# Kernel tuning notes

Measured on AMD Instinct MI355X. Metric: run time of the kernel, lower is better.

Reference implementation:

```python
import jax, jax.numpy as jnp
import numpy as np

N = 100_000          # nodes (node_shape = [N, D])
D = 64               # node feature dim
E = 3_200_000        # edges (edge_shape = [E, 1]), avg degree 32
GAMMA = 0.5          # registered buffer 'gamma'


def setup_inputs() -> dict:
    key = jax.random.key(0)
    k1, k2, k3, k4 = jax.random.split(key, 4)
    h = jax.random.normal(k1, (N * D,), dtype=jnp.float32)
    e = jax.random.normal(k2, (E,), dtype=jnp.float32)
    x = jnp.concatenate([h, e])                      # flat ODE state [N*D + E]
    src = jax.random.randint(k3, (E,), 0, N, dtype=jnp.int32)
    dst = jax.random.randint(k4, (E,), 0, N, dtype=jnp.int32)
    t = jnp.zeros((1,), dtype=jnp.float32)           # unused by the math
    return {"t": t, "x": x, "src": src, "dst": dst}


def reference(t, x, src, dst):
    # split flat state into node features and edge weights
    h = x[: N * D].reshape(N, D)        # ndata['h']
    e = x[N * D:].reshape(E, 1)         # edata['e']
    h0 = h
    # update_all(u_mul_e('h','e','m'), sum('m','h')):
    # gather source features, scale by edge weight, scatter-sum to dst
    msgs = h[src] * e                                   # [E, D]
    h_agg = jax.ops.segment_sum(msgs, dst, num_segments=N)  # [N, D]
    h_new = h_agg - h0 * GAMMA
    # self.h0 is None -> no residual add
    return jnp.concatenate([h_new.reshape(-1), jnp.zeros((E,), x.dtype)])
```

## Files before the change

kernel.cpp:

```cpp
#include <hip/hip_runtime.h>

#define N_NODES 100000
#define D_FEAT  64
#define N_EDGES 3200000
#define GAMMA   0.5f

#define BSH   7
#define BN    (1 << BSH)
#define NB    ((N_NODES + BN - 1) >> BSH)
#define CH    2048
#define NC    ((N_EDGES + CH - 1) / CH)

#define Z_BLOCKS   782
#define CVT_V4     (N_NODES * D_FEAT / 4)
#define CVT_BLOCKS ((CVT_V4 + 255) / 256)

#define KG_REG   10
#define KG_CAP   4736
#define SRC_MASK 0x1FFFFu

__global__ void __launch_bounds__(256)
p0_kernel(const float* __restrict__ h,
          const int* __restrict__ dst,
          unsigned short* __restrict__ h16,
          unsigned short* __restrict__ mat,
          float* __restrict__ out_edge) {
    __shared__ int hist[NB];
    const int bid = blockIdx.x;
    const int t   = threadIdx.x;
    if (bid < NC) {
        for (int i = t; i < NB; i += 256) hist[i] = 0;
        __syncthreads();
        const int base  = bid * CH;
        const int chcnt = min(N_EDGES - base, CH);
        const int4* dst4 = (const int4*)(dst + base);
        const int nv4 = chcnt >> 2;
#pragma unroll
        for (int j = 0; j < 2; ++j) {
            int i = j * 256 + t;
            if (i < nv4) {
                int4 d = dst4[i];
                __hip_atomic_fetch_add(&hist[d.x >> BSH], 1, __ATOMIC_RELAXED, __HIP_MEMORY_SCOPE_WORKGROUP);
                __hip_atomic_fetch_add(&hist[d.y >> BSH], 1, __ATOMIC_RELAXED, __HIP_MEMORY_SCOPE_WORKGROUP);
                __hip_atomic_fetch_add(&hist[d.z >> BSH], 1, __ATOMIC_RELAXED, __HIP_MEMORY_SCOPE_WORKGROUP);
                __hip_atomic_fetch_add(&hist[d.w >> BSH], 1, __ATOMIC_RELAXED, __HIP_MEMORY_SCOPE_WORKGROUP);
            }
        }
        __syncthreads();
        for (int i = t; i < NB; i += 256)
            mat[bid * NB + i] = (unsigned short)hist[i];
    } else if (bid < NC + Z_BLOCKS) {
        float4* oe4 = (float4*)out_edge;
        const int b2 = bid - NC;
        const float4 z = make_float4(0.f, 0.f, 0.f, 0.f);
#pragma unroll
        for (int j = 0; j < 4; ++j) {
            int i = b2 * 1024 + j * 256 + t;
            if (i < N_EDGES / 4) oe4[i] = z;
        }
    } else {
        int i = (bid - NC - Z_BLOCKS) * 256 + t;
        if (i < CVT_V4) {
            float4 v = ((const float4*)h)[i];
            ushort4 o;
            unsigned u;
            u = __float_as_uint(v.x); o.x = (unsigned short)((u + 0x7fffu + ((u >> 16) & 1u)) >> 16);
            u = __float_as_uint(v.y); o.y = (unsigned short)((u + 0x7fffu + ((u >> 16) & 1u)) >> 16);
            u = __float_as_uint(v.z); o.z = (unsigned short)((u + 0x7fffu + ((u >> 16) & 1u)) >> 16);
            u = __float_as_uint(v.w); o.w = (unsigned short)((u + 0x7fffu + ((u >> 16) & 1u)) >> 16);
            ((ushort4*)h16)[i] = o;
        }
    }
}

__global__ void __launch_bounds__(64)
matscan_kernel(unsigned short* __restrict__ mat,
               int* __restrict__ rowsum) {
    const int b = blockIdx.x;
    const int l = threadIdx.x;
    int carry = 0;
    for (int r = 0; r < (NC + 63) / 64; ++r) {
        int c = r * 64 + l;
        int v = (c < NC) ? (int)mat[c * NB + b] : 0;
        int incl = v;
        for (int s = 1; s < 64; s <<= 1) {
            int u = __shfl_up(incl, s, 64);
            if (l >= s) incl += u;
        }
        if (c < NC) mat[c * NB + b] = (unsigned short)(carry + incl - v);
        carry += __shfl(incl, 63, 64);
    }
    if (l == 0) rowsum[b] = carry;
}

__global__ void __launch_bounds__(512)
bucket_scatter_kernel(const int* __restrict__ src,
                      const int* __restrict__ dst,
                      const float* __restrict__ e,
                      const unsigned short* __restrict__ mat,
                      const int* __restrict__ rowsum,
                      int* __restrict__ offs_g,
                      uint2* __restrict__ recs) {
    __shared__ uint2          stage[CH];
    __shared__ unsigned short bkt[CH];
    __shared__ int hist[NB], ebuf[NB], pos[NB], diff[NB];
    __shared__ int offsL[NB + 1];
    __shared__ int wsum[8];

    const int t    = threadIdx.x;
    const int lane = t & 63;
    const int wid  = t >> 6;
    const int c    = blockIdx.x;
    const int base = c * CH;
    const int chcnt = min(N_EDGES - base, CH);
    const int i0 = 2 * t, i1 = 2 * t + 1;

    for (int i = t; i < NB; i += 512) hist[i] = 0;
    int a  = (i0 < NB) ? rowsum[i0] : 0;
    int d1 = (i1 < NB) ? rowsum[i1] : 0;
    int pair = a + d1, incl = pair;
    for (int s = 1; s < 64; s <<= 1) {
        int u = __shfl_up(incl, s, 64);
        if (lane >= s) incl += u;
    }
    if (lane == 63) wsum[wid] = incl;
    __syncthreads();
    {
        int pre = 0;
        for (int w = 0; w < wid; ++w) pre += wsum[w];
        int excl = pre + incl - pair;
        if (i0 < NB) offsL[i0] = excl;
        if (i1 < NB) offsL[i1] = excl + a;
        if (t == 511) offsL[NB] = pre + incl;
    }
    int dv[4];
#pragma unroll
    for (int j = 0; j < 4; ++j) {
        int i = j * 512 + t;
        if (i < chcnt) {
            dv[j] = dst[base + i];
            __hip_atomic_fetch_add(&hist[dv[j] >> BSH], 1,
                                   __ATOMIC_RELAXED, __HIP_MEMORY_SCOPE_WORKGROUP);
        } else dv[j] = -1;
    }
    __syncthreads();
    int c0 = (i0 < NB) ? hist[i0] : 0;
    int c1 = (i1 < NB) ? hist[i1] : 0;
    int p2 = c0 + c1, incl2 = p2;
    for (int s = 1; s < 64; s <<= 1) {
        int u = __shfl_up(incl2, s, 64);
        if (lane >= s) incl2 += u;
    }
    if (lane == 63) wsum[wid] = incl2;
    __syncthreads();
    {
        int pre = 0;
        for (int w = 0; w < wid; ++w) pre += wsum[w];
        int excl2 = pre + incl2 - p2;
        if (i0 < NB) {
            ebuf[i0] = excl2;
            pos[i0]  = excl2;
            diff[i0] = offsL[i0] + (int)mat[c * NB + i0] - excl2;
        }
        if (i1 < NB) {
            ebuf[i1] = excl2 + c0;
            pos[i1]  = excl2 + c0;
            diff[i1] = offsL[i1] + (int)mat[c * NB + i1] - (excl2 + c0);
        }
    }
    __syncthreads();
#pragma unroll
    for (int j = 0; j < 4; ++j) {
        if (dv[j] >= 0) {
            int gi = base + j * 512 + t;
            int b  = dv[j] >> BSH;
            int p  = __hip_atomic_fetch_add(&pos[b], 1,
                            __ATOMIC_RELAXED, __HIP_MEMORY_SCOPE_WORKGROUP);
            unsigned pk = (unsigned)src[gi] | ((unsigned)(dv[j] & (BN - 1)) << 17);
            stage[p] = make_uint2(pk, __float_as_uint(e[gi]));
            bkt[p]   = (unsigned short)b;
        }
    }
    __syncthreads();
    for (int i = t; i < chcnt; i += 512) {
        recs[diff[bkt[i]] + i] = stage[i];
    }
    if (c == 0) {
        for (int i = t; i <= NB; i += 512) offs_g[i] = offsL[i];
    }
}

__global__ void __launch_bounds__(512)
sort_gather_kernel(const float* __restrict__ h,
                   const unsigned short* __restrict__ h16,
                   const int* __restrict__ offs,
                   const uint2* __restrict__ recs,
                   float* __restrict__ out) {
    __shared__ uint2 kw[KG_CAP];
    __shared__ int hist[BN], ebuf[BN], pos[BN];
    __shared__ int wsum[2];

    const int b    = blockIdx.x;
    const int t    = threadIdx.x;
    const int lane = t & 63;
    const int wid  = t >> 6;
    const int g    = lane >> 3;
    const int sub  = lane & 7;
    const int lo   = offs[b];
    const int cnt  = offs[b + 1] - lo;

    const uint4* __restrict__ hv = (const uint4*)h16;

#define ACC_KW(kx, wx)                                                      \
    {                                                                       \
        uint4 v = hv[((kx) & SRC_MASK) * 8 + sub];                          \
        a0 += __uint_as_float(v.x << 16) * (wx);                            \
        a1 += __uint_as_float(v.x & 0xFFFF0000u) * (wx);                    \
        a2 += __uint_as_float(v.y << 16) * (wx);                            \
        a3 += __uint_as_float(v.y & 0xFFFF0000u) * (wx);                    \
        a4 += __uint_as_float(v.z << 16) * (wx);                            \
        a5 += __uint_as_float(v.z & 0xFFFF0000u) * (wx);                    \
        a6 += __uint_as_float(v.w << 16) * (wx);                            \
        a7 += __uint_as_float(v.w & 0xFFFF0000u) * (wx);                    \
    }

    if (cnt <= KG_CAP) {
        if (t < BN) hist[t] = 0;
        __syncthreads();
        uint2 r[KG_REG];
#pragma unroll
        for (int j = 0; j < KG_REG; ++j) {
            int i = j * 512 + t;
            if (i < cnt) {
                r[j] = recs[lo + i];
                __hip_atomic_fetch_add(&hist[r[j].x >> 17], 1,
                                       __ATOMIC_RELAXED, __HIP_MEMORY_SCOPE_WORKGROUP);
            } else r[j].x = 0xFFFFFFFFu;
        }
        __syncthreads();
        int c = 0, incl = 0;
        if (t < BN) { c = hist[t]; incl = c; }
        for (int s = 1; s < 64; s <<= 1) {
            int u = __shfl_up(incl, s, 64);
            if (lane >= s) incl += u;
        }
        if (t < BN && lane == 63) wsum[wid] = incl;
        __syncthreads();
        if (t < BN) {
            int pre = (wid == 1) ? wsum[0] : 0;
            int exc = pre + incl - c;
            ebuf[t] = exc;
            pos[t]  = exc;
        }
        __syncthreads();
#pragma unroll
        for (int j = 0; j < KG_REG; ++j) {
            if (r[j].x != 0xFFFFFFFFu) {
                int dl = r[j].x >> 17;
                int p  = __hip_atomic_fetch_add(&pos[dl], 1,
                                __ATOMIC_RELAXED, __HIP_MEMORY_SCOPE_WORKGROUP);
                kw[p] = r[j];
            }
        }
        __syncthreads();
        for (int i = 0; i < 16; ++i) {
            const int ln  = wid * 16 + i;
            const int n   = (b << BSH) + ln;
            const int nlo = ebuf[ln];
            const int nhi = pos[ln];
            float a0=0.f,a1=0.f,a2=0.f,a3=0.f,a4=0.f,a5=0.f,a6=0.f,a7=0.f;
            int kk = nlo + g;
            while (kk < nhi) {
                uint2 q0 = kw[kk];
                bool m1 = kk +  8 < nhi;
                bool m2 = kk + 16 < nhi;
                bool m3 = kk + 24 < nhi;
                uint2 q1 = m1 ? kw[kk +  8] : make_uint2(0u, 0u);
                uint2 q2 = m2 ? kw[kk + 16] : make_uint2(0u, 0u);
                uint2 q3 = m3 ? kw[kk + 24] : make_uint2(0u, 0u);
                ACC_KW(q0.x, __uint_as_float(q0.y));
                ACC_KW(q1.x, __uint_as_float(q1.y));
                ACC_KW(q2.x, __uint_as_float(q2.y));
                ACC_KW(q3.x, __uint_as_float(q3.y));
                kk += 32;
            }
            for (int m = 8; m <= 32; m <<= 1) {
                a0 += __shfl_xor(a0, m); a1 += __shfl_xor(a1, m);
                a2 += __shfl_xor(a2, m); a3 += __shfl_xor(a3, m);
                a4 += __shfl_xor(a4, m); a5 += __shfl_xor(a5, m);
                a6 += __shfl_xor(a6, m); a7 += __shfl_xor(a7, m);
            }
            if (g == 0 && n < N_NODES) {
                const float4* __restrict__ h4 = (const float4*)h;
                const int o = n * 16 + sub * 2;
                float4 p = h4[o], q = h4[o + 1];
                float4 r0, r1;
                r0.x = a0 - GAMMA * p.x; r0.y = a1 - GAMMA * p.y;
                r0.z = a2 - GAMMA * p.z; r0.w = a3 - GAMMA * p.w;
                r1.x = a4 - GAMMA * q.x; r1.y = a5 - GAMMA * q.y;
                r1.z = a6 - GAMMA * q.z; r1.w = a7 - GAMMA * q.w;
                ((float4*)out)[o]     = r0;
                ((float4*)out)[o + 1] = r1;
            }
        }
    } else {
        for (int i = 0; i < 16; ++i) {
            const int ln = wid * 16 + i;
            const int n  = (b << BSH) + ln;
            float a0=0.f,a1=0.f,a2=0.f,a3=0.f,a4=0.f,a5=0.f,a6=0.f,a7=0.f;
            for (int k = lo + g; k < lo + cnt; k += 8) {
                uint2 rr = recs[k];
                if ((int)(rr.x >> 17) == ln) ACC_KW(rr.x, __uint_as_float(rr.y));
            }
            for (int m = 8; m <= 32; m <<= 1) {
                a0 += __shfl_xor(a0, m); a1 += __shfl_xor(a1, m);
                a2 += __shfl_xor(a2, m); a3 += __shfl_xor(a3, m);
                a4 += __shfl_xor(a4, m); a5 += __shfl_xor(a5, m);
                a6 += __shfl_xor(a6, m); a7 += __shfl_xor(a7, m);
            }
            if (g == 0 && n < N_NODES) {
                const float4* __restrict__ h4 = (const float4*)h;
                const int o = n * 16 + sub * 2;
                float4 p = h4[o], q = h4[o + 1];
                float4 r0, r1;
                r0.x = a0 - GAMMA * p.x; r0.y = a1 - GAMMA * p.y;
                r0.z = a2 - GAMMA * p.z; r0.w = a3 - GAMMA * p.w;
                r1.x = a4 - GAMMA * q.x; r1.y = a5 - GAMMA * q.y;
                r1.z = a6 - GAMMA * q.z; r1.w = a7 - GAMMA * q.w;
                ((float4*)out)[o]     = r0;
                ((float4*)out)[o + 1] = r1;
            }
        }
    }
#undef ACC_KW
}

__global__ void init_out_kernel(const float* __restrict__ x,
                                float* __restrict__ out,
                                int nd, int total) {
    int i = blockIdx.x * blockDim.x + threadIdx.x;
    if (i < nd)         out[i] = -GAMMA * x[i];
    else if (i < total) out[i] = 0.0f;
}

__global__ void edge_scatter_kernel(const float* __restrict__ h,
                                    const float* __restrict__ e,
                                    const int* __restrict__ src,
                                    const int* __restrict__ dst,
                                    float* __restrict__ out) {
    long long idx = (long long)blockIdx.x * blockDim.x + threadIdx.x;
    int edge = (int)(idx >> 6);
    int d    = (int)(idx & 63);
    if (edge >= N_EDGES) return;
    atomicAdd(&out[dst[edge] * D_FEAT + d], h[src[edge] * D_FEAT + d] * e[edge]);
}

extern "C" void kernel_launch(void* const* d_in, const int* in_sizes, int n_in,
                              void* d_out, int out_size, void* d_ws, size_t ws_size,
                              hipStream_t stream) {
    const float* x   = (const float*)d_in[1];
    const int*   src = (const int*)d_in[2];
    const int*   dst = (const int*)d_in[3];
    float*       out = (float*)d_out;

    const int nd = N_NODES * D_FEAT;

    size_t ints    = (size_t)(NB + 1) + NB;
    size_t mat_off = ints * 4;
    size_t rec_off = (mat_off + (size_t)NC * NB * 2 + 255) & ~(size_t)255;
    size_t h16_off = (rec_off + (size_t)N_EDGES * 8 + 255) & ~(size_t)255;
    size_t needed  = h16_off + (size_t)nd * 2;

    if (ws_size >= needed) {
        int* offs   = (int*)d_ws;
        int* rowsum = offs + NB + 1;
        unsigned short* mat  = (unsigned short*)((char*)d_ws + mat_off);
        uint2*          recs = (uint2*)((char*)d_ws + rec_off);
        unsigned short* h16  = (unsigned short*)((char*)d_ws + h16_off);

        p0_kernel<<<NC + Z_BLOCKS + CVT_BLOCKS, 256, 0, stream>>>(
            x, dst, h16, mat, out + nd);
        matscan_kernel<<<NB, 64, 0, stream>>>(mat, rowsum);
        bucket_scatter_kernel<<<NC, 512, 0, stream>>>(
            src, dst, x + nd, mat, rowsum, offs, recs);
        sort_gather_kernel<<<NB, 512, 0, stream>>>(x, h16, offs, recs, out);
    } else {
        const int total = nd + N_EDGES;
        init_out_kernel<<<(total + 255) / 256, 256, 0, stream>>>(x, out, nd, total);
        long long threads = (long long)N_EDGES * 64;
        edge_scatter_kernel<<<(int)((threads + 255) / 256), 256, 0, stream>>>(
            x, x + nd, src, dst, out);
    }
}
```

Before: 128.5 us.

## Halve destination bucket size to 64 nodes and rework scans for doubled buckets

Bucket width drops from 128 to 64 destination nodes, which doubles the bucket count to about 1563 and halves per-bucket edge capacity, so the gather kernel gets twice as many smaller blocks with lower LDS use. The bucket scatter kernel now scans four buckets per thread and reuses its histogram array as the position counter, dropping the ebuf and pos arrays to fit LDS. The gather kernel's bucket-local scan collapses to a single wave and drops one barrier. The trade-off is a larger count matrix and heavier scans in the pre-pass and scatter kernels.

```diff
diff --git a/kernel.cpp b/kernel.cpp
--- a/kernel.cpp
+++ b/kernel.cpp
@@ -5,7 +5,7 @@
 #define N_EDGES 3200000
 #define GAMMA   0.5f
 
-#define BSH   7
+#define BSH   6
 #define BN    (1 << BSH)
 #define NB    ((N_NODES + BN - 1) >> BSH)
 #define CH    2048
@@ -15,8 +15,8 @@
 #define CVT_V4     (N_NODES * D_FEAT / 4)
 #define CVT_BLOCKS ((CVT_V4 + 255) / 256)
 
-#define KG_REG   10
-#define KG_CAP   4736
+#define KG_REG   5
+#define KG_CAP   2368
 #define SRC_MASK 0x1FFFFu
 
 __global__ void __launch_bounds__(256)
@@ -103,7 +103,8 @@
                       uint2* __restrict__ recs) {
     __shared__ uint2          stage[CH];
     __shared__ unsigned short bkt[CH];
-    __shared__ int hist[NB], ebuf[NB], pos[NB], diff[NB];
+    __shared__ int hist[NB];
+    __shared__ int diff[NB];
     __shared__ int offsL[NB + 1];
     __shared__ int wsum[8];
 
@@ -113,12 +114,14 @@
     const int c    = blockIdx.x;
     const int base = c * CH;
     const int chcnt = min(N_EDGES - base, CH);
-    const int i0 = 2 * t, i1 = 2 * t + 1;
+    const int q0 = 4 * t, q1 = q0 + 1, q2 = q0 + 2, q3 = q0 + 3;
 
     for (int i = t; i < NB; i += 512) hist[i] = 0;
-    int a  = (i0 < NB) ? rowsum[i0] : 0;
-    int d1 = (i1 < NB) ? rowsum[i1] : 0;
-    int pair = a + d1, incl = pair;
+    int a0 = (q0 < NB) ? rowsum[q0] : 0;
+    int a1 = (q1 < NB) ? rowsum[q1] : 0;
+    int a2 = (q2 < NB) ? rowsum[q2] : 0;
+    int a3 = (q3 < NB) ? rowsum[q3] : 0;
+    int s4 = a0 + a1 + a2 + a3, incl = s4;
     for (int s = 1; s < 64; s <<= 1) {
         int u = __shfl_up(incl, s, 64);
         if (lane >= s) incl += u;
@@ -128,9 +131,11 @@
     {
         int pre = 0;
         for (int w = 0; w < wid; ++w) pre += wsum[w];
-        int excl = pre + incl - pair;
-        if (i0 < NB) offsL[i0] = excl;
-        if (i1 < NB) offsL[i1] = excl + a;
+        int exc = pre + incl - s4;
+        if (q0 < NB) offsL[q0] = exc;
+        if (q1 < NB) offsL[q1] = exc + a0;
+        if (q2 < NB) offsL[q2] = exc + a0 + a1;
+        if (q3 < NB) offsL[q3] = exc + a0 + a1 + a2;
         if (t == 511) offsL[NB] = pre + incl;
     }
     int dv[4];
@@ -144,9 +149,11 @@
         } else dv[j] = -1;
     }
     __syncthreads();
-    int c0 = (i0 < NB) ? hist[i0] : 0;
-    int c1 = (i1 < NB) ? hist[i1] : 0;
-    int p2 = c0 + c1, incl2 = p2;
+    int c0 = (q0 < NB) ? hist[q0] : 0;
+    int c1 = (q1 < NB) ? hist[q1] : 0;
+    int c2 = (q2 < NB) ? hist[q2] : 0;
+    int c3 = (q3 < NB) ? hist[q3] : 0;
+    int t4 = c0 + c1 + c2 + c3, incl2 = t4;
     for (int s = 1; s < 64; s <<= 1) {
         int u = __shfl_up(incl2, s, 64);
         if (lane >= s) incl2 += u;
@@ -156,17 +163,12 @@
     {
         int pre = 0;
         for (int w = 0; w < wid; ++w) pre += wsum[w];
-        int excl2 = pre + incl2 - p2;
-        if (i0 < NB) {
-            ebuf[i0] = excl2;
-            pos[i0]  = excl2;
-            diff[i0] = offsL[i0] + (int)mat[c * NB + i0] - excl2;
-        }
-        if (i1 < NB) {
-            ebuf[i1] = excl2 + c0;
-            pos[i1]  = excl2 + c0;
-            diff[i1] = offsL[i1] + (int)mat[c * NB + i1] - (excl2 + c0);
-        }
+        int e0 = pre + incl2 - t4;
+        int e1 = e0 + c0, e2 = e1 + c1, e3 = e2 + c2;
+        if (q0 < NB) { hist[q0] = e0; diff[q0] = offsL[q0] + (int)mat[c * NB + q0] - e0; }
+        if (q1 < NB) { hist[q1] = e1; diff[q1] = offsL[q1] + (int)mat[c * NB + q1] - e1; }
+        if (q2 < NB) { hist[q2] = e2; diff[q2] = offsL[q2] + (int)mat[c * NB + q2] - e2; }
+        if (q3 < NB) { hist[q3] = e3; diff[q3] = offsL[q3] + (int)mat[c * NB + q3] - e3; }
     }
     __syncthreads();
 #pragma unroll
@@ -174,7 +176,7 @@
         if (dv[j] >= 0) {
             int gi = base + j * 512 + t;
             int b  = dv[j] >> BSH;
-            int p  = __hip_atomic_fetch_add(&pos[b], 1,
+            int p  = __hip_atomic_fetch_add(&hist[b], 1,
                             __ATOMIC_RELAXED, __HIP_MEMORY_SCOPE_WORKGROUP);
             unsigned pk = (unsigned)src[gi] | ((unsigned)(dv[j] & (BN - 1)) << 17);
             stage[p] = make_uint2(pk, __float_as_uint(e[gi]));
@@ -198,7 +200,6 @@
                    float* __restrict__ out) {
     __shared__ uint2 kw[KG_CAP];
     __shared__ int hist[BN], ebuf[BN], pos[BN];
-    __shared__ int wsum[2];
 
     const int b    = blockIdx.x;
     const int t    = threadIdx.x;
@@ -238,17 +239,13 @@
             } else r[j].x = 0xFFFFFFFFu;
         }
         __syncthreads();
-        int c = 0, incl = 0;
-        if (t < BN) { c = hist[t]; incl = c; }
-        for (int s = 1; s < 64; s <<= 1) {
-            int u = __shfl_up(incl, s, 64);
-            if (lane >= s) incl += u;
-        }
-        if (t < BN && lane == 63) wsum[wid] = incl;
-        __syncthreads();
         if (t < BN) {
-            int pre = (wid == 1) ? wsum[0] : 0;
-            int exc = pre + incl - c;
+            int c = hist[t], incl = c;
+            for (int s = 1; s < 64; s <<= 1) {
+                int u = __shfl_up(incl, s, 64);
+                if (lane >= s) incl += u;
+            }
+            int exc = incl - c;
             ebuf[t] = exc;
             pos[t]  = exc;
         }
@@ -263,8 +260,8 @@
             }
         }
         __syncthreads();
-        for (int i = 0; i < 16; ++i) {
-            const int ln  = wid * 16 + i;
+        for (int i = 0; i < 8; ++i) {
+            const int ln  = wid * 8 + i;
             const int n   = (b << BSH) + ln;
             const int nlo = ebuf[ln];
             const int nhi = pos[ln];
@@ -304,8 +301,8 @@
             }
         }
     } else {
-        for (int i = 0; i < 16; ++i) {
-            const int ln = wid * 16 + i;
+        for (int i = 0; i < 8; ++i) {
+            const int ln = wid * 8 + i;
             const int n  = (b << BSH) + ln;
             float a0=0.f,a1=0.f,a2=0.f,a3=0.f,a4=0.f,a5=0.f,a6=0.f,a7=0.f;
             for (int k = lo + g; k < lo + cnt; k += 8) {
```

After: 138.9 us. +8.1%, slower.
